# Performance work log

Hardware: AMD Instinct MI355X
Metric: run time of the kernel (lower is better)

## Reference

```python
import jax, jax.numpy as jnp
import numpy as np

N = 80000      # nodes (spots)
D = 1000       # input_dim (genes)
E = 1280000    # edges (avg degree 16)
FH1, FH2 = 64, 16
GH1, GH2 = 64, 16
K = 10         # dec_cluster_n
ALPHA = 1.0
MASK = int(0.8 * N)
BN_EPS = 1e-3


def _xavier(key, shape):
    fan_in, fan_out = shape[0], shape[1]
    lim = jnp.sqrt(6.0 / (fan_in + fan_out))
    return jax.random.uniform(key, shape, jnp.float32, -lim, lim)


def setup_inputs() -> dict:
    key = jax.random.key(0)
    ks = jax.random.split(key, 32)
    x = jax.random.normal(ks[0], (N, D), jnp.float32)
    edge_rows = jax.random.randint(ks[1], (E,), 0, N, jnp.int32)
    edge_cols = jax.random.randint(ks[2], (E,), 0, N, jnp.int32)
    edge_vals = jax.random.uniform(ks[3], (E,), jnp.float32)
    mask_nodes = jax.random.permutation(ks[4], N)[:MASK].astype(jnp.int32)
    enc_mask_token = 0.02 * jax.random.normal(ks[5], (1, D), jnp.float32)
    # encoder L1: Linear + BatchNorm (eval: running stats)
    W1 = _xavier(ks[6], (D, FH1)); b1 = jnp.zeros((FH1,), jnp.float32)
    g1 = jnp.ones((FH1,), jnp.float32); be1 = jnp.zeros((FH1,), jnp.float32)
    rm1 = 0.1 * jax.random.normal(ks[7], (FH1,), jnp.float32)
    rv1 = 0.5 + jax.random.uniform(ks[8], (FH1,), jnp.float32)
    # encoder L2
    W2 = _xavier(ks[9], (FH1, FH2)); b2 = jnp.zeros((FH2,), jnp.float32)
    g2 = jnp.ones((FH2,), jnp.float32); be2 = jnp.zeros((FH2,), jnp.float32)
    rm2 = 0.1 * jax.random.normal(ks[10], (FH2,), jnp.float32)
    rv2 = 0.5 + jax.random.uniform(ks[11], (FH2,), jnp.float32)
    # GCN weights
    Wgc1 = _xavier(ks[12], (FH2, GH1))
    Wgc2 = _xavier(ks[13], (GH1, GH2))
    Wgc3 = _xavier(ks[14], (GH1, GH2))
    Wdec = _xavier(ks[15], (GH2 + FH2, D))
    cluster_layer = jax.random.normal(ks[16], (K, GH2 + FH2), jnp.float32) * jnp.sqrt(2.0 / (K + GH2 + FH2))
    return dict(x=x, edge_rows=edge_rows, edge_cols=edge_cols, edge_vals=edge_vals,
                mask_nodes=mask_nodes, enc_mask_token=enc_mask_token,
                W1=W1, b1=b1, g1=g1, be1=be1, rm1=rm1, rv1=rv1,
                W2=W2, b2=b2, g2=g2, be2=be2, rm2=rm2, rv2=rv2,
                Wgc1=Wgc1, Wgc2=Wgc2, Wgc3=Wgc3, Wdec=Wdec,
                cluster_layer=cluster_layer)


def _bn_eval(h, g, b, rm, rv):
    return (h - rm) * (g * jax.lax.rsqrt(rv + BN_EPS)) + b


def _spmm(rows, cols, vals, dense):
    # sparse adj [N,N] @ dense [N,F]
    return jax.ops.segment_sum(vals[:, None] * dense[cols], rows, num_segments=N)


def _l2norm(v):
    n = jnp.sqrt(jnp.sum(v * v, axis=-1, keepdims=True))
    return v / jnp.maximum(n, 1e-12)


def reference(x, edge_rows, edge_cols, edge_vals, mask_nodes, enc_mask_token,
              W1, b1, g1, be1, rm1, rv1, W2, b2, g2, be2, rm2, rv2,
              Wgc1, Wgc2, Wgc3, Wdec, cluster_layer):
    # encoding_mask_noise: add mask token to masked nodes (eval: dropout off)
    out_x = x.at[mask_nodes].add(enc_mask_token[0])
    # dense encoder (Linear -> BN(eval) -> ELU; dropout off)
    h = jax.nn.elu(_bn_eval(out_x @ W1 + b1, g1, be1, rm1, rv1))
    feat_x = jax.nn.elu(_bn_eval(h @ W2 + b2, g2, be2, rm2, rv2))
    # GCN layers: mm then spmm
    hidden1 = jax.nn.relu(_spmm(edge_rows, edge_cols, edge_vals, feat_x @ Wgc1))
    mu = _spmm(edge_rows, edge_cols, edge_vals, hidden1 @ Wgc2)
    logvar = _spmm(edge_rows, edge_cols, edge_vals, hidden1 @ Wgc3)
    gnn_z = mu  # eval-mode reparameterize
    z = jnp.concatenate([feat_x, gnn_z], axis=1)  # [N, 32]
    de_feat = _spmm(edge_rows, edge_cols, edge_vals, z @ Wdec)  # identity act
    # student-t cluster soft assignments
    d2 = jnp.sum(jnp.square(z[:, None, :] - cluster_layer[None, :, :]), axis=2)  # [N,K]
    q = 1.0 / (1.0 + d2 / ALPHA)
    q = q ** ((ALPHA + 1.0) / 2.0)
    q = q / jnp.sum(q, axis=1, keepdims=True)
    # sce loss on masked nodes
    x_init = out_x[mask_nodes]
    x_rec = de_feat[mask_nodes]
    loss = jnp.mean((1.0 - jnp.sum(_l2norm(x_rec) * _l2norm(x_init), axis=-1)) ** 3)
    return (z, mu, logvar, de_feat, q, feat_x, gnn_z, loss)
```

## Files before the change

kernel.cpp:

```cpp
#include <hip/hip_runtime.h>
#include <hip/hip_bf16.h>
#include <math.h>

#define Nn 80000
#define Dd 1000
#define Ee 1280000
#define MM 64000
#define NT 32

typedef __attribute__((ext_vector_type(8))) short bf16x8;
typedef __attribute__((ext_vector_type(4))) float f32x4;

__device__ inline unsigned short f2bf(float f){
  union { float f; unsigned u; } c; c.f = f;
  unsigned u = c.u;
  u += 0x7FFFu + ((u >> 16) & 1u);
  return (unsigned short)(u >> 16);
}
__device__ inline float bf2f(unsigned short s){
  return __uint_as_float(((unsigned)s) << 16);
}

__device__ __forceinline__ void gload16(const void* g, void* l){
  __builtin_amdgcn_global_load_lds(
      (const __attribute__((address_space(1))) void*)g,
      (__attribute__((address_space(3))) void*)l, 16, 0, 0);
}

__device__ __forceinline__ bf16x8 cvt8(f32x4 a, f32x4 b){
  union { __hip_bfloat162 h; unsigned u; } c0, c1, c2, c3;
  c0.h = __float22bfloat162_rn(make_float2(a.x, a.y));
  c1.h = __float22bfloat162_rn(make_float2(a.z, a.w));
  c2.h = __float22bfloat162_rn(make_float2(b.x, b.y));
  c3.h = __float22bfloat162_rn(make_float2(b.z, b.w));
  union { unsigned u[4]; bf16x8 v; } r;
  r.u[0] = c0.u; r.u[1] = c1.u; r.u[2] = c2.u; r.u[3] = c3.u;
  return r.v;
}

__global__ __launch_bounds__(256) void k_init(const float* __restrict__ W1,
    const float* __restrict__ Wdec, const float* __restrict__ token,
    unsigned short* __restrict__ Wim, unsigned short* __restrict__ WdT2,
    float* __restrict__ tw, int* __restrict__ flags, int* __restrict__ deg,
    float* __restrict__ loss)
{
  int i = blockIdx.x*256 + threadIdx.x;
  if (i < 131072){
    int t   = i >> 12;
    int rem = i & 4095;
    int c   = rem >> 5;
    int pos = rem & 31;
    int slot = pos >> 3;
    int j    = pos & 7;
    int u    = slot ^ (c & 3);
    int k    = t*32 + u*8 + j;
    float v = 0.f;
    if (c < 96 && k < Dd) v = (c < 64) ? W1[k*64 + c] : Wdec[(size_t)(c-64)*Dd + k];
    Wim[i] = f2bf(v);
  }
  unsigned t1 = (unsigned)(i - 131072);
  if (t1 < 32768u){
    int col = t1 >> 5, k = t1 & 31;
    WdT2[t1] = (col < Dd) ? f2bf(Wdec[(size_t)k*Dd + col]) : (unsigned short)0;
  }
  if (i < Nn){ flags[i] = 0; deg[i] = 0; }
  if (i == 0) *loss = 0.f;
  unsigned u3 = (unsigned)(i - 163840);
  if (u3 < 6208u){
    int j = u3 >> 6, l = u3 & 63;
    float s = 0.f;
    if (j < 64){ for (int k = l; k < Dd; k += 64) s += token[k]*W1[k*64 + j]; }
    else if (j < 96){ const float* wr = Wdec + (size_t)(j-64)*Dd;
                      for (int k = l; k < Dd; k += 64) s += token[k]*wr[k]; }
    else { for (int k = l; k < Dd; k += 64) s += token[k]*token[k]; }
    #pragma unroll
    for (int o = 32; o; o >>= 1) s += __shfl_down(s, o);
    if (l == 0) tw[j] = s;
  }
}

__global__ __launch_bounds__(256) void k_flags(const int* __restrict__ mask,
    int* __restrict__ flags)
{
  int i = blockIdx.x*256 + threadIdx.x;
  if (i < MM) flags[mask[i]] = 1;
}

__global__ __launch_bounds__(256, 4) void k_gemm1(
    const float* __restrict__ x, const unsigned short* __restrict__ Wim,
    const int* __restrict__ flags, const float* __restrict__ tw,
    const float* __restrict__ token,
    const float* __restrict__ b1, const float* __restrict__ g1,
    const float* __restrict__ be1, const float* __restrict__ rm1,
    const float* __restrict__ rv1, const float* __restrict__ W2,
    const float* __restrict__ b2, const float* __restrict__ g2,
    const float* __restrict__ be2, const float* __restrict__ rm2,
    const float* __restrict__ rv2, float* __restrict__ fx,
    float* __restrict__ wx, float* __restrict__ sii_node,
    const int* __restrict__ erow, const int* __restrict__ ecol,
    const float* __restrict__ evls, int* __restrict__ deg,
    int2* __restrict__ buck)
{
  __shared__ char smem[37888];
  if (blockIdx.x >= 625){
    int i = (blockIdx.x - 625)*256 + threadIdx.x;
    if (i < Ee){
      int r = erow[i];
      int s = atomicAdd(&deg[r], 1);
      if (s < 64){
        int2 pr; pr.x = ecol[i]; pr.y = __float_as_int(evls[i]);
        buck[((size_t)r << 6) + s] = pr;
      }
    }
    return;
  }
  unsigned short* As = (unsigned short*)smem;
  float* tokL = (float*)(smem + 24576);
  const int tid  = threadIdx.x;
  const int lane = tid & 63;
  const int wave = tid >> 6;
  const int wm = wave >> 1, wn = wave & 1;
  const int l15 = lane & 15, kg = lane >> 4;
  const int row0 = blockIdx.x * 128;

  const int rtid = tid >> 3;
  const int kq   = (tid & 7) * 4;
  const int wu   = (kq >> 3) ^ (rtid & 3) ^ ((rtid >> 2) & 3);
  const int wofs = rtid*32 + wu*8 + (kq & 4);

  const float* xbase = x + (size_t)row0 * Dd;
  f32x4 ra[4];

  for (int i = tid; i < 1024; i += 256) tokL[i] = (i < Dd) ? token[i] : 0.f;

  {
    int col = kq;
    #pragma unroll
    for (int j = 0; j < 4; ++j)
      ra[j] = *(const f32x4*)(xbase + (size_t)(j*32 + rtid)*Dd + col);
    const char* wim = (const char*)Wim;
    gload16(wim + (wave*2  )*1024 + lane*16, smem + 8192 + (wave*2  )*1024);
    gload16(wim + (wave*2+1)*1024 + lane*16, smem + 8192 + (wave*2+1)*1024);
  }
  asm volatile("s_waitcnt lgkmcnt(0)" ::: "memory");
  __builtin_amdgcn_s_barrier();

  const f32x4 zero4 = {0.f,0.f,0.f,0.f};
  f32x4 acc[4][3];
  #pragma unroll
  for (int i = 0; i < 4; ++i){ acc[i][0]=zero4; acc[i][1]=zero4; acc[i][2]=zero4; }
  float sx2[4] = {0.f,0.f,0.f,0.f};
  float sxt[4] = {0.f,0.f,0.f,0.f};

  #pragma unroll 2
  for (int t = 0; t < NT; ++t){
    const char* Bb = smem + 8192 + (t&1)*8192;
    const int k0 = t*32;
    const bool kok = (t < NT-1) || (kq <= 4);
    f32x4 tok4 = *(const f32x4*)(tokL + k0 + kq);

    #pragma unroll
    for (int j = 0; j < 4; ++j){
      f32x4 v = ra[j];
      if (kok){
        sx2[j] += v.x*v.x + v.y*v.y + v.z*v.z + v.w*v.w;
        sxt[j] += v.x*tok4.x + v.y*tok4.y + v.z*tok4.z + v.w*tok4.w;
      }
      union { __hip_bfloat162 h; unsigned u; } c0, c1;
      c0.h = __float22bfloat162_rn(make_float2(v.x, v.y));
      c1.h = __float22bfloat162_rn(make_float2(v.z, v.w));
      uint2 pk; pk.x = c0.u; pk.y = c1.u;
      *reinterpret_cast<uint2*>(&As[j*1024 + wofs]) = pk;
    }

    if (t + 1 < NT){
      int col = k0 + 32 + kq; if (col > 996) col = 996;
      #pragma unroll
      for (int j = 0; j < 4; ++j)
        ra[j] = *(const f32x4*)(xbase + (size_t)(j*32 + rtid)*Dd + col);
      const char* wim = (const char*)Wim + (size_t)(t+1)*8192;
      char* Bn = smem + 8192 + ((t+1)&1)*8192;
      gload16(wim + (wave*2  )*1024 + lane*16, Bn + (wave*2  )*1024);
      gload16(wim + (wave*2+1)*1024 + lane*16, Bn + (wave*2+1)*1024);
      asm volatile("s_waitcnt lgkmcnt(0)" ::: "memory");
      asm volatile("s_waitcnt vmcnt(6)" ::: "memory");
    } else {
      asm volatile("s_waitcnt lgkmcnt(0)" ::: "memory");
      asm volatile("s_waitcnt vmcnt(0)" ::: "memory");
    }
    __builtin_amdgcn_s_barrier();
    __builtin_amdgcn_sched_barrier(0);

    bf16x8 bfr[3];
    #pragma unroll
    for (int ni = 0; ni < 3; ++ni){
      int c = wn*48 + ni*16 + l15;
      bfr[ni] = *(const bf16x8*)(Bb + c*64 + ((kg ^ (c & 3)) << 4));
    }
    const int ru = (kg ^ (l15 & 3) ^ ((l15 >> 2) & 3)) << 4;
    #pragma unroll
    for (int mi = 0; mi < 4; ++mi){
      int r = wm*64 + mi*16 + l15;
      bf16x8 af = *(const bf16x8*)((const char*)As + r*64 + ru);
      acc[mi][0] = __builtin_amdgcn_mfma_f32_16x16x32_bf16(af, bfr[0], acc[mi][0], 0, 0, 0);
      acc[mi][1] = __builtin_amdgcn_mfma_f32_16x16x32_bf16(af, bfr[1], acc[mi][1], 0, 0, 0);
      acc[mi][2] = __builtin_amdgcn_mfma_f32_16x16x32_bf16(af, bfr[2], acc[mi][2], 0, 0, 0);
    }
    __builtin_amdgcn_sched_barrier(0);
    __builtin_amdgcn_s_barrier();
  }

  float stt = tw[96];
  #pragma unroll
  for (int j = 0; j < 4; ++j){
    float a2 = sx2[j], at = sxt[j];
    a2 += __shfl_xor(a2, 1); at += __shfl_xor(at, 1);
    a2 += __shfl_xor(a2, 2); at += __shfl_xor(at, 2);
    a2 += __shfl_xor(a2, 4); at += __shfl_xor(at, 4);
    if ((tid & 7) == 0){
      int row = row0 + j*32 + rtid;
      float fl = flags[row] ? 1.f : 0.f;
      sii_node[row] = a2 + fl*(2.f*at + stt);
    }
  }

  float flv[4][4];
  #pragma unroll
  for (int mi = 0; mi < 4; ++mi)
    #pragma unroll
    for (int r4 = 0; r4 < 4; ++r4)
      flv[mi][r4] = flags[row0 + wm*64 + mi*16 + (lane>>4)*4 + r4] ? 1.f : 0.f;

  float* Hs  = (float*)smem;
  float* W2s = (float*)(smem + 33792);
  for (int i = tid; i < 1024; i += 256) W2s[i] = W2[i];

  #pragma unroll
  for (int ni = 0; ni < 3; ++ni){
    int n = wn*48 + ni*16 + l15;
    float twn = tw[n];
    if (n < 64){
      float bb = b1[n], rmv = rm1[n];
      float scv = g1[n]*rsqrtf(rv1[n] + 1e-3f), bev = be1[n];
      #pragma unroll
      for (int mi = 0; mi < 4; ++mi){
        #pragma unroll
        for (int r4 = 0; r4 < 4; ++r4){
          int lrow = wm*64 + mi*16 + (lane>>4)*4 + r4;
          float v = (acc[mi][ni][r4] + flv[mi][r4]*twn + bb - rmv)*scv + bev;
          v = (v > 0.f) ? v : expm1f(v);
          Hs[lrow*66 + n] = v;
        }
      }
    } else {
      int j = n - 64;
      #pragma unroll
      for (int mi = 0; mi < 4; ++mi){
        #pragma unroll
        for (int r4 = 0; r4 < 4; ++r4){
          int lrow = wm*64 + mi*16 + (lane>>4)*4 + r4;
          wx[(size_t)(row0 + lrow)*32 + j] = acc[mi][ni][r4] + flv[mi][r4]*twn;
        }
      }
    }
  }
  __syncthreads();

  {
    int j = tid & 15;
    float pb = b2[j], prm = rm2[j];
    float psc = g2[j]*rsqrtf(rv2[j] + 1e-3f), pbe = be2[j];
    int rb = (tid >> 4) * 8;
    #pragma unroll
    for (int rr = 0; rr < 8; ++rr){
      int r = rb + rr;
      float a = pb;
      #pragma unroll
      for (int k = 0; k < 64; ++k) a += Hs[r*66 + k]*W2s[k*16 + j];
      float v = (a - prm)*psc + pbe;
      v = (v > 0.f) ? v : expm1f(v);
      fx[(size_t)(row0 + r)*16 + j] = v;
    }
  }
}

__global__ __launch_bounds__(256) void k_spmm16(const int* __restrict__ deg,
    const int2* __restrict__ buck, const float* __restrict__ in,
    float* __restrict__ out, const float* __restrict__ Wgc1,
    unsigned short* __restrict__ h1b)
{
  __shared__ float Ws[1024];
  for (int t = threadIdx.x; t < 1024; t += 256) Ws[t] = Wgc1[t];
  __syncthreads();
  int row = blockIdx.x*16 + (threadIdx.x >> 4);
  int l = threadIdx.x & 15;
  int d = deg[row]; if (d > 64) d = 64;
  const int2* bp = buck + ((size_t)row << 6);
  float acc = 0.f;
  for (int p = 0; p < d; ++p){
    int2 ce = bp[p];
    acc += __int_as_float(ce.y) * in[(size_t)ce.x*16 + l];
  }
  out[(size_t)row*16 + l] = acc;
  float h0=0.f, h1=0.f, h2=0.f, h3=0.f;
  #pragma unroll
  for (int k = 0; k < 16; ++k){
    float av = __shfl(acc, k, 16);
    const float* wp = &Ws[k*64 + l*4];
    h0 += av*wp[0]; h1 += av*wp[1]; h2 += av*wp[2]; h3 += av*wp[3];
  }
  ushort4 pk;
  pk.x = f2bf(fmaxf(h0, 0.f)); pk.y = f2bf(fmaxf(h1, 0.f));
  pk.z = f2bf(fmaxf(h2, 0.f)); pk.w = f2bf(fmaxf(h3, 0.f));
  *reinterpret_cast<ushort4*>(&h1b[(size_t)row*64 + l*4]) = pk;
}

__global__ __launch_bounds__(256) void k_gcn2(const int* __restrict__ deg,
    const int2* __restrict__ buck, const unsigned short* __restrict__ h1b,
    const float* __restrict__ Wgc2, const float* __restrict__ Wgc3,
    const float* __restrict__ fx, const float* __restrict__ cl,
    float* __restrict__ z, float* __restrict__ mu,
    float* __restrict__ lv, float* __restrict__ gz, float* __restrict__ q)
{
  __shared__ float ah[16][65];
  __shared__ float Ws[2048];
  __shared__ float cls[320];
  __shared__ float zs[16][33];
  __shared__ float qv[16][10];
  int t = threadIdx.x;
  for (int i = t; i < 1024; i += 256){ Ws[i] = Wgc2[i]; Ws[1024 + i] = Wgc3[i]; }
  for (int i = t; i < 320; i += 256) cls[i] = cl[i];
  const int wave = t >> 6, lane = t & 63;
  const int row0 = blockIdx.x*16;
  #pragma unroll
  for (int rr = 0; rr < 4; ++rr){
    int lr = wave*4 + rr;
    int row = row0 + lr;
    int d = deg[row]; if (d > 64) d = 64;
    const int2* bp = buck + ((size_t)row << 6);
    float acc = 0.f;
    for (int p = 0; p < d; ++p){
      int2 ce = bp[p];
      acc += __int_as_float(ce.y) * bf2f(h1b[(size_t)ce.x*64 + lane]);
    }
    ah[lr][lane] = acc;
  }
  __syncthreads();
  {
    int r = t >> 4, j = t & 15;
    const float* ar = ah[r];
    float m = 0.f, l = 0.f;
    #pragma unroll 16
    for (int k = 0; k < 64; ++k){
      float a = ar[k];
      m += a*Ws[k*16 + j];
      l += a*Ws[1024 + k*16 + j];
    }
    size_t grow = (size_t)(row0 + r);
    mu[grow*16 + j] = m;
    gz[grow*16 + j] = m;
    z[grow*32 + 16 + j] = m;
    zs[r][16 + j] = m;
    lv[grow*16 + j] = l;
    float v = fx[grow*16 + j];
    z[grow*32 + j] = v;
    zs[r][j] = v;
  }
  __syncthreads();
  if (t < 160){
    int r = t / 10, c = t - r*10;
    float d2 = 0.f;
    #pragma unroll
    for (int k = 0; k < 32; ++k){ float d = zs[r][k] - cls[c*32 + k]; d2 += d*d; }
    qv[r][c] = 1.f/(1.f + d2);
  }
  __syncthreads();
  if (t < 160){
    int r = t / 10, c = t - r*10;
    float ss = 0.f;
    #pragma unroll
    for (int cc = 0; cc < 10; ++cc) ss += qv[r][cc];
    q[(size_t)(row0 + r)*10 + c] = qv[r][c]/ss;
  }
}

__global__ __launch_bounds__(256) void k_dec(const float* __restrict__ afx,
    const float* __restrict__ mu, const int* __restrict__ deg,
    const int2* __restrict__ buck, const unsigned short* __restrict__ WdT2,
    const float* __restrict__ wx, const float* __restrict__ sii_node,
    const int* __restrict__ flags, float* __restrict__ de,
    float* __restrict__ loss)
{
  __shared__ float stg[4][16][68];
  __shared__ float amuL[64][17];
  __shared__ float bsum[4];
  const int tid  = threadIdx.x;
  const int lane = tid & 63;
  const int wave = tid >> 6;
  const int base = blockIdx.x*64;

  {
    int l = tid & 15, rg = tid >> 4;
    #pragma unroll
    for (int pass = 0; pass < 4; ++pass){
      int lr = pass*16 + rg;
      int row = base + lr;
      int d = deg[row]; if (d > 64) d = 64;
      const int2* bp = buck + ((size_t)row << 6);
      float acc = 0.f;
      for (int p = 0; p < d; ++p){
        int2 ce = bp[p];
        acc += __int_as_float(ce.y) * mu[(size_t)ce.x*16 + l];
      }
      amuL[lr][l] = acc;
    }
  }
  __syncthreads();

  const int r0 = base + wave*16;
  const int kg = lane >> 4;
  const int l15 = lane & 15;
  const int row = r0 + l15;
  f32x4 a0, a1;
  if (kg < 2){
    const float* asrc = afx + (size_t)row*16 + kg*8;
    a0 = *reinterpret_cast<const f32x4*>(asrc);
    a1 = *reinterpret_cast<const f32x4*>(asrc + 4);
  } else {
    const float* asrc = &amuL[wave*16 + l15][(kg-2)*8];
    a0 = *reinterpret_cast<const f32x4*>(asrc);
    a1 = *reinterpret_cast<const f32x4*>(asrc + 4);
  }
  bf16x8 af = cvt8(a0, a1);
  const float* wsrc = wx + (size_t)row*32 + kg*8;
  f32x4 w0 = *reinterpret_cast<const f32x4*>(wsrc);
  f32x4 w1 = *reinterpret_cast<const f32x4*>(wsrc + 4);
  float sri = a0.x*w0.x + a0.y*w0.y + a0.z*w0.z + a0.w*w0.w
            + a1.x*w1.x + a1.y*w1.y + a1.z*w1.z + a1.w*w1.w;

  const f32x4 zero4 = {0.f,0.f,0.f,0.f};
  float sq = 0.f;
  float (*S)[68] = stg[wave];
  const int srow = lane >> 4;
  const int scol = l15*4;

  for (int g = 0; g < 16; ++g){
    int c0 = g*64;
    #pragma unroll
    for (int j = 0; j < 4; ++j){
      int cb = c0 + j*16;
      bf16x8 bf = *reinterpret_cast<const bf16x8*>(&WdT2[(size_t)(cb + l15)*32 + kg*8]);
      f32x4 d = __builtin_amdgcn_mfma_f32_16x16x32_bf16(bf, af, zero4, 0, 0, 0);
      sq += d[0]*d[0] + d[1]*d[1] + d[2]*d[2] + d[3]*d[3];
      *reinterpret_cast<f32x4*>(&S[l15][j*16 + kg*4]) = d;
    }
    asm volatile("s_waitcnt lgkmcnt(0)" ::: "memory");
    __builtin_amdgcn_sched_barrier(0);
    #pragma unroll
    for (int sub = 0; sub < 4; ++sub){
      int lr = sub*4 + srow;
      int cc = c0 + scol;
      if (cc < Dd){
        f32x4 v = *reinterpret_cast<const f32x4*>(&S[lr][scol]);
        *reinterpret_cast<f32x4*>(&de[(size_t)(r0 + lr)*Dd + cc]) = v;
      }
    }
    __builtin_amdgcn_sched_barrier(0);
    asm volatile("s_waitcnt lgkmcnt(0)" ::: "memory");
  }
  sq  += __shfl_xor(sq, 16);  sq  += __shfl_xor(sq, 32);
  sri += __shfl_xor(sri, 16); sri += __shfl_xor(sri, 32);
  float tval = 0.f;
  if (kg == 0){
    float nr = fmaxf(sqrtf(sq), 1e-12f);
    float ni = fmaxf(sqrtf(sii_node[row]), 1e-12f);
    float tt = 1.f - sri/(nr*ni);
    tval = flags[row] ? tt*tt*tt : 0.f;
  }
  #pragma unroll
  for (int o = 1; o < 16; o <<= 1) tval += __shfl_xor(tval, o);
  if (lane == 0) bsum[wave] = tval;
  __syncthreads();
  if (tid == 0)
    atomicAdd(loss, (bsum[0] + bsum[1] + bsum[2] + bsum[3]) * (1.f/MM));
}

extern "C" void kernel_launch(void* const* d_in, const int* in_sizes, int n_in,
                              void* d_out, int out_size, void* d_ws, size_t ws_size,
                              hipStream_t stream)
{
  const float* x     = (const float*)d_in[0];
  const int*   erow  = (const int*)  d_in[1];
  const int*   ecol  = (const int*)  d_in[2];
  const float* evls  = (const float*)d_in[3];
  const int*   mask  = (const int*)  d_in[4];
  const float* token = (const float*)d_in[5];
  const float* W1  = (const float*)d_in[6];
  const float* b1  = (const float*)d_in[7];
  const float* g1  = (const float*)d_in[8];
  const float* be1 = (const float*)d_in[9];
  const float* rm1 = (const float*)d_in[10];
  const float* rv1 = (const float*)d_in[11];
  const float* W2  = (const float*)d_in[12];
  const float* b2  = (const float*)d_in[13];
  const float* g2  = (const float*)d_in[14];
  const float* be2 = (const float*)d_in[15];
  const float* rm2 = (const float*)d_in[16];
  const float* rv2 = (const float*)d_in[17];
  const float* Wgc1= (const float*)d_in[18];
  const float* Wgc2= (const float*)d_in[19];
  const float* Wgc3= (const float*)d_in[20];
  const float* Wdec= (const float*)d_in[21];
  const float* clus= (const float*)d_in[22];

  float* out = (float*)d_out;
  float* oz  = out;
  float* omu = out + (size_t)Nn*32;
  float* olv = omu + (size_t)Nn*16;
  float* ode = olv + (size_t)Nn*16;
  float* oq  = ode + (size_t)Nn*1000;
  float* ofx = oq  + (size_t)Nn*10;
  float* ogz = ofx + (size_t)Nn*16;
  float* olo = ogz + (size_t)Nn*16;

  char* w = (char*)d_ws;
  unsigned short* Wim  = (unsigned short*)w; w += (size_t)262144;
  unsigned short* WdT2 = (unsigned short*)w; w += (size_t)65536;
  float* tw    = (float*)w; w += 512;
  int* flags   = (int*)w;   w += (size_t)Nn*4;
  int* deg     = (int*)w;   w += (size_t)Nn*4;
  int2* buck   = (int2*)w;  w += (size_t)Nn*64*8;
  float* afx   = (float*)w; w += (size_t)Nn*16*4;
  unsigned short* h1b = (unsigned short*)w; w += (size_t)Nn*64*2;
  float* wx    = (float*)w; w += (size_t)Nn*32*4;
  float* sii   = (float*)w; w += (size_t)Nn*4;

  k_init<<<dim3(665), dim3(256), 0, stream>>>(W1, Wdec, token, Wim, WdT2, tw,
      flags, deg, olo);
  k_flags<<<dim3((MM+255)/256), dim3(256), 0, stream>>>(mask, flags);
  k_gemm1<<<dim3(5625), dim3(256), 0, stream>>>(x, Wim, flags, tw, token,
      b1, g1, be1, rm1, rv1, W2, b2, g2, be2, rm2, rv2, ofx, wx, sii,
      erow, ecol, evls, deg, buck);
  k_spmm16<<<dim3(Nn/16), dim3(256), 0, stream>>>(deg, buck, ofx, afx, Wgc1, h1b);
  k_gcn2<<<dim3(Nn/16), dim3(256), 0, stream>>>(deg, buck, h1b, Wgc2, Wgc3,
      ofx, clus, oz, omu, olv, ogz, oq);
  k_dec<<<dim3(Nn/64), dim3(256), 0, stream>>>(afx, omu, deg, buck, WdT2,
      wx, sii, flags, ode, olo);
}
```

Baseline: 485.8 us.

## Double-buffer A tile in encoder GEMM and store decoder output directly

The encoder GEMM now double-buffers the bf16 A tile in LDS alongside B. The next tile is converted and written while MFMAs run on the current one, leaving one barrier per iteration instead of two. The decoder stops staging MFMA results through LDS and writes each lane's 4-float fragment straight to global memory. That removes the LDS round trip and its waits, but makes the global stores less coalesced: 16-byte writes scattered across rows.

```diff
diff --git a/kernel.cpp b/kernel.cpp
--- a/kernel.cpp
+++ b/kernel.cpp
@@ -114,8 +114,7 @@
     }
     return;
   }
-  unsigned short* As = (unsigned short*)smem;
-  float* tokL = (float*)(smem + 24576);
+  float* tokL = (float*)(smem + 32768);
   const int tid  = threadIdx.x;
   const int lane = tid & 63;
   const int wave = tid >> 6;
@@ -134,62 +133,79 @@
   for (int i = tid; i < 1024; i += 256) tokL[i] = (i < Dd) ? token[i] : 0.f;
 
   {
-    int col = kq;
     #pragma unroll
     for (int j = 0; j < 4; ++j)
-      ra[j] = *(const f32x4*)(xbase + (size_t)(j*32 + rtid)*Dd + col);
+      ra[j] = *(const f32x4*)(xbase + (size_t)(j*32 + rtid)*Dd + kq);
     const char* wim = (const char*)Wim;
-    gload16(wim + (wave*2  )*1024 + lane*16, smem + 8192 + (wave*2  )*1024);
-    gload16(wim + (wave*2+1)*1024 + lane*16, smem + 8192 + (wave*2+1)*1024);
-  }
-  asm volatile("s_waitcnt lgkmcnt(0)" ::: "memory");
-  __builtin_amdgcn_s_barrier();
-
-  const f32x4 zero4 = {0.f,0.f,0.f,0.f};
-  f32x4 acc[4][3];
-  #pragma unroll
-  for (int i = 0; i < 4; ++i){ acc[i][0]=zero4; acc[i][1]=zero4; acc[i][2]=zero4; }
+    gload16(wim + (wave*2  )*1024 + lane*16, smem + 16384 + (wave*2  )*1024);
+    gload16(wim + (wave*2+1)*1024 + lane*16, smem + 16384 + (wave*2+1)*1024);
+  }
+  __syncthreads();
+
   float sx2[4] = {0.f,0.f,0.f,0.f};
   float sxt[4] = {0.f,0.f,0.f,0.f};
 
-  #pragma unroll 2
-  for (int t = 0; t < NT; ++t){
-    const char* Bb = smem + 8192 + (t&1)*8192;
-    const int k0 = t*32;
-    const bool kok = (t < NT-1) || (kq <= 4);
-    f32x4 tok4 = *(const f32x4*)(tokL + k0 + kq);
-
+  {
+    unsigned short* An = (unsigned short*)smem;
+    f32x4 tok4 = *(const f32x4*)(tokL + kq);
     #pragma unroll
     for (int j = 0; j < 4; ++j){
       f32x4 v = ra[j];
-      if (kok){
-        sx2[j] += v.x*v.x + v.y*v.y + v.z*v.z + v.w*v.w;
-        sxt[j] += v.x*tok4.x + v.y*tok4.y + v.z*tok4.z + v.w*tok4.w;
-      }
+      sx2[j] += v.x*v.x + v.y*v.y + v.z*v.z + v.w*v.w;
+      sxt[j] += v.x*tok4.x + v.y*tok4.y + v.z*tok4.z + v.w*tok4.w;
       union { __hip_bfloat162 h; unsigned u; } c0, c1;
       c0.h = __float22bfloat162_rn(make_float2(v.x, v.y));
       c1.h = __float22bfloat162_rn(make_float2(v.z, v.w));
       uint2 pk; pk.x = c0.u; pk.y = c1.u;
-      *reinterpret_cast<uint2*>(&As[j*1024 + wofs]) = pk;
-    }
+      *reinterpret_cast<uint2*>(&An[j*1024 + wofs]) = pk;
+    }
+    #pragma unroll
+    for (int j = 0; j < 4; ++j)
+      ra[j] = *(const f32x4*)(xbase + (size_t)(j*32 + rtid)*Dd + 32 + kq);
+  }
+  asm volatile("s_waitcnt lgkmcnt(0)" ::: "memory");
+  asm volatile("s_waitcnt vmcnt(4)" ::: "memory");
+  __builtin_amdgcn_s_barrier();
+  __builtin_amdgcn_sched_barrier(0);
+
+  const f32x4 zero4 = {0.f,0.f,0.f,0.f};
+  f32x4 acc[4][3];
+  #pragma unroll
+  for (int i = 0; i < 4; ++i){ acc[i][0]=zero4; acc[i][1]=zero4; acc[i][2]=zero4; }
+
+  #pragma unroll 2
+  for (int t = 0; t < NT; ++t){
+    const char* Ab = smem + (t&1)*8192;
+    const char* Bb = smem + 16384 + (t&1)*8192;
 
     if (t + 1 < NT){
-      int col = k0 + 32 + kq; if (col > 996) col = 996;
-      #pragma unroll
-      for (int j = 0; j < 4; ++j)
-        ra[j] = *(const f32x4*)(xbase + (size_t)(j*32 + rtid)*Dd + col);
       const char* wim = (const char*)Wim + (size_t)(t+1)*8192;
-      char* Bn = smem + 8192 + ((t+1)&1)*8192;
+      char* Bn = smem + 16384 + ((t+1)&1)*8192;
       gload16(wim + (wave*2  )*1024 + lane*16, Bn + (wave*2  )*1024);
       gload16(wim + (wave*2+1)*1024 + lane*16, Bn + (wave*2+1)*1024);
-      asm volatile("s_waitcnt lgkmcnt(0)" ::: "memory");
-      asm volatile("s_waitcnt vmcnt(6)" ::: "memory");
-    } else {
-      asm volatile("s_waitcnt lgkmcnt(0)" ::: "memory");
-      asm volatile("s_waitcnt vmcnt(0)" ::: "memory");
-    }
-    __builtin_amdgcn_s_barrier();
-    __builtin_amdgcn_sched_barrier(0);
+      unsigned short* An = (unsigned short*)(smem + ((t+1)&1)*8192);
+      const bool kok = (t+1 < NT-1) || (kq <= 4);
+      f32x4 tok4 = *(const f32x4*)(tokL + (t+1)*32 + kq);
+      #pragma unroll
+      for (int j = 0; j < 4; ++j){
+        f32x4 v = ra[j];
+        if (kok){
+          sx2[j] += v.x*v.x + v.y*v.y + v.z*v.z + v.w*v.w;
+          sxt[j] += v.x*tok4.x + v.y*tok4.y + v.z*tok4.z + v.w*tok4.w;
+        }
+        union { __hip_bfloat162 h; unsigned u; } c0, c1;
+        c0.h = __float22bfloat162_rn(make_float2(v.x, v.y));
+        c1.h = __float22bfloat162_rn(make_float2(v.z, v.w));
+        uint2 pk; pk.x = c0.u; pk.y = c1.u;
+        *reinterpret_cast<uint2*>(&An[j*1024 + wofs]) = pk;
+      }
+      if (t + 2 < NT){
+        int col = (t+2)*32 + kq; if (col > 996) col = 996;
+        #pragma unroll
+        for (int j = 0; j < 4; ++j)
+          ra[j] = *(const f32x4*)(xbase + (size_t)(j*32 + rtid)*Dd + col);
+      }
+    }
 
     bf16x8 bfr[3];
     #pragma unroll
@@ -201,13 +217,17 @@
     #pragma unroll
     for (int mi = 0; mi < 4; ++mi){
       int r = wm*64 + mi*16 + l15;
-      bf16x8 af = *(const bf16x8*)((const char*)As + r*64 + ru);
+      bf16x8 af = *(const bf16x8*)(Ab + r*64 + ru);
       acc[mi][0] = __builtin_amdgcn_mfma_f32_16x16x32_bf16(af, bfr[0], acc[mi][0], 0, 0, 0);
       acc[mi][1] = __builtin_amdgcn_mfma_f32_16x16x32_bf16(af, bfr[1], acc[mi][1], 0, 0, 0);
       acc[mi][2] = __builtin_amdgcn_mfma_f32_16x16x32_bf16(af, bfr[2], acc[mi][2], 0, 0, 0);
     }
+
+    asm volatile("s_waitcnt lgkmcnt(0)" ::: "memory");
+    if (t < NT-2) asm volatile("s_waitcnt vmcnt(4)" ::: "memory");
+    else          asm volatile("s_waitcnt vmcnt(0)" ::: "memory");
+    __builtin_amdgcn_s_barrier();
     __builtin_amdgcn_sched_barrier(0);
-    __builtin_amdgcn_s_barrier();
   }
 
   float stt = tw[96];
@@ -391,7 +411,6 @@
     const int* __restrict__ flags, float* __restrict__ de,
     float* __restrict__ loss)
 {
-  __shared__ float stg[4][16][68];
   __shared__ float amuL[64][17];
   __shared__ float bsum[4];
   const int tid  = threadIdx.x;
@@ -440,10 +459,8 @@
 
   const f32x4 zero4 = {0.f,0.f,0.f,0.f};
   float sq = 0.f;
-  float (*S)[68] = stg[wave];
-  const int srow = lane >> 4;
-  const int scol = l15*4;
-
+  float* drow = de + (size_t)row*Dd;
+  #pragma unroll 4
   for (int g = 0; g < 16; ++g){
     int c0 = g*64;
     #pragma unroll
@@ -452,21 +469,10 @@
       bf16x8 bf = *reinterpret_cast<const bf16x8*>(&WdT2[(size_t)(cb + l15)*32 + kg*8]);
       f32x4 d = __builtin_amdgcn_mfma_f32_16x16x32_bf16(bf, af, zero4, 0, 0, 0);
       sq += d[0]*d[0] + d[1]*d[1] + d[2]*d[2] + d[3]*d[3];
-      *reinterpret_cast<f32x4*>(&S[l15][j*16 + kg*4]) = d;
-    }
-    asm volatile("s_waitcnt lgkmcnt(0)" ::: "memory");
-    __builtin_amdgcn_sched_barrier(0);
-    #pragma unroll
-    for (int sub = 0; sub < 4; ++sub){
-      int lr = sub*4 + srow;
-      int cc = c0 + scol;
-      if (cc < Dd){
-        f32x4 v = *reinterpret_cast<const f32x4*>(&S[lr][scol]);
-        *reinterpret_cast<f32x4*>(&de[(size_t)(r0 + lr)*Dd + cc]) = v;
-      }
-    }
-    __builtin_amdgcn_sched_barrier(0);
-    asm volatile("s_waitcnt lgkmcnt(0)" ::: "memory");
+      int cc = cb + kg*4;
+      if (cc < Dd)
+        *reinterpret_cast<f32x4*>(drow + cc) = d;
+    }
   }
   sq  += __shfl_xor(sq, 16);  sq  += __shfl_xor(sq, 32);
   sri += __shfl_xor(sri, 16); sri += __shfl_xor(sri, 32);
```

Measured after the change: 502.0 us. 1.03x slower.
